# Optimization experiments

Hardware: AMD Instinct MI355X
Metric: run time of the kernel (lower is better)

## Reference

```python
import jax, jax.numpy as jnp
import numpy as np

D_MODEL = 1024
NUM_HEADS = 16


def setup_inputs() -> dict:
    key = jax.random.key(0)
    kx, kq, kk, kv, ko = jax.random.split(key, 5)
    B, S, D = 4, 2048, D_MODEL
    scale = 0.02
    x = jax.random.normal(kx, (B, S, D), dtype=jnp.float32)
    wq = jax.random.normal(kq, (D, D), dtype=jnp.float32) * scale
    wk = jax.random.normal(kk, (D, D), dtype=jnp.float32) * scale
    wv = jax.random.normal(kv, (D, D), dtype=jnp.float32) * scale
    wo = jax.random.normal(ko, (D, D), dtype=jnp.float32) * scale
    return {"x": x, "wq": wq, "wk": wk, "wv": wv, "wo": wo}


def reference(x, wq, wk, wv, wo):
    B, S, D = x.shape
    H = NUM_HEADS
    dk = D // H
    # projections: weight is [out, in] -> y = x @ W^T
    q = jnp.einsum('bsd,ed->bse', x, wq).reshape(B, S, H, dk).transpose(0, 2, 1, 3)
    k = jnp.einsum('bsd,ed->bse', x, wk).reshape(B, S, H, dk).transpose(0, 2, 1, 3)
    v = jnp.einsum('bsd,ed->bse', x, wv).reshape(B, S, H, dk).transpose(0, 2, 1, 3)
    # scaled dot-product attention with causal mask, [B,H,S,S]
    scores = jnp.einsum('bhqd,bhkd->bhqk', q, k) / jnp.sqrt(jnp.asarray(dk, x.dtype))
    causal = jnp.tril(jnp.ones((S, S), dtype=bool))
    scores = jnp.where(causal, scores, -jnp.inf)
    attn = jax.nn.softmax(scores, axis=-1)
    out = jnp.einsum('bhqk,bhkd->bhqd', attn, v)
    out = out.transpose(0, 2, 1, 3).reshape(B, S, D)
    return jnp.einsum('bse,de->bsd', out, wo)
```

## Files before the change

kernel.cpp:

```cpp
#include <hip/hip_runtime.h>

#define SEQ 2048
#define DM 1024
#define NH 16
#define DKH 64

typedef __attribute__((ext_vector_type(8))) short short8;
typedef __attribute__((ext_vector_type(4))) float f32x4;
typedef __attribute__((ext_vector_type(16))) float f32x16;
typedef __attribute__((ext_vector_type(2))) unsigned int u32x2;
typedef __attribute__((ext_vector_type(4))) unsigned int u32x4;

static __device__ __forceinline__ unsigned short f2b(float f) {
  unsigned int u = __float_as_uint(f);
  u += 0x7fffu + ((u >> 16) & 1u);
  return (unsigned short)(u >> 16);
}

static __device__ __forceinline__ short8 ldfrag_bf(const unsigned short* p) {
  return *reinterpret_cast<const short8*>(p);
}
static __device__ __forceinline__ short8 ldfrag_f32(const float* p) {
  const float4* q = reinterpret_cast<const float4*>(p);
  float4 a = q[0], b = q[1];
  short8 r;
  r[0] = (short)f2b(a.x); r[1] = (short)f2b(a.y);
  r[2] = (short)f2b(a.z); r[3] = (short)f2b(a.w);
  r[4] = (short)f2b(b.x); r[5] = (short)f2b(b.y);
  r[6] = (short)f2b(b.z); r[7] = (short)f2b(b.w);
  return r;
}

static __device__ __forceinline__ void gl_lds16(const void* g, void* l) {
  __builtin_amdgcn_global_load_lds(
      (const __attribute__((address_space(1))) unsigned int*)g,
      (__attribute__((address_space(3))) unsigned int*)l, 16, 0, 0);
}

__global__ __launch_bounds__(256) void zero_f32(float* __restrict__ p, int n4) {
  int i = blockIdx.x * 256 + threadIdx.x;
  if (i < n4) {
    float4 z = {0.f, 0.f, 0.f, 0.f};
    reinterpret_cast<float4*>(p)[i] = z;
  }
}

__global__ __launch_bounds__(256) void cast_all(const float* __restrict__ x,
                                                const float* __restrict__ a, const float* __restrict__ b,
                                                const float* __restrict__ c, const float* __restrict__ d,
                                                unsigned short* __restrict__ xo,
                                                unsigned short* __restrict__ oa, unsigned short* __restrict__ ob,
                                                unsigned short* __restrict__ oc, unsigned short* __restrict__ od) {
  int blk = blockIdx.x;
  if (blk < 8192) {
    int i = blk * 256 + threadIdx.x;
    float4 v = reinterpret_cast<const float4*>(x)[i];
    ushort4 o;
    o.x = f2b(v.x); o.y = f2b(v.y); o.z = f2b(v.z); o.w = f2b(v.w);
    reinterpret_cast<ushort4*>(xo)[i] = o;
  } else {
    blk -= 8192;
    int which = blk >> 10;
    int i = (blk & 1023) * 256 + threadIdx.x;
    const float* s = (which == 0) ? a : (which == 1) ? b : (which == 2) ? c : d;
    unsigned short* o = (which == 0) ? oa : (which == 1) ? ob : (which == 2) ? oc : od;
    float sc = (which == 0) ? 0.125f : 1.0f;
    float4 v = reinterpret_cast<const float4*>(s)[i];
    ushort4 u;
    u.x = f2b(v.x * sc); u.y = f2b(v.y * sc); u.z = f2b(v.z * sc); u.w = f2b(v.w * sc);
    reinterpret_cast<ushort4*>(o)[i] = u;
  }
}

__global__ __launch_bounds__(256) void gemm_qkv(const unsigned short* __restrict__ A,
                                                const unsigned short* __restrict__ Wq,
                                                const unsigned short* __restrict__ Wk,
                                                const unsigned short* __restrict__ Wv,
                                                unsigned short* __restrict__ Qb,
                                                unsigned short* __restrict__ Kb,
                                                unsigned short* __restrict__ Vt) {
  __shared__ char smem[49152];
  unsigned short* At = (unsigned short*)smem;
  unsigned short* Wt = (unsigned short*)(smem + 24576);
  int t = threadIdx.x;
  int lane = t & 63;
  int w = t >> 6;
  int l16 = lane & 15, q4 = lane >> 4;
  int mode = blockIdx.x % 3;
  int bid = blockIdx.x / 3;
  int mt = bid >> 3, nt = bid & 7;
  int m0 = mt * 128, n0 = nt * 128;
  int mw = (w & 1) * 64, nw = (w >> 1) * 64;
  const unsigned short* W = (mode == 0) ? Wq : (mode == 1) ? Wk : Wv;

  const f32x4 zero4 = {0.f, 0.f, 0.f, 0.f};
  f32x4 acc[4][4];
#pragma unroll
  for (int mi = 0; mi < 4; ++mi)
#pragma unroll
    for (int nj = 0; nj < 4; ++nj) acc[mi][nj] = zero4;

  int rl0 = t >> 2, cp = t & 3;
  int rl1 = rl0 + 64;
  int sw0 = ((cp - rl0 - (rl0 >> 2)) & 3) * 8;
  int sw1 = ((cp - rl1 - (rl1 >> 2)) & 3) * 8;
  const unsigned short* ga0 = A + (long)(m0 + rl0) * DM + sw0;
  const unsigned short* ga1 = A + (long)(m0 + rl1) * DM + sw1;
  const unsigned short* gw0 = W + (long)(n0 + rl0) * DM + sw0;
  const unsigned short* gw1 = W + (long)(n0 + rl1) * DM + sw1;
  char* lA = (char*)At + t * 16;
  char* lW = (char*)Wt + t * 16;

  int aoff[4], woff[4];
#pragma unroll
  for (int mi = 0; mi < 4; ++mi) {
    int r = mw + mi * 16 + l16;
    aoff[mi] = r * 32 + ((q4 + r + (r >> 2)) & 3) * 8;
  }
#pragma unroll
  for (int nj = 0; nj < 4; ++nj) {
    int r = nw + nj * 16 + l16;
    woff[nj] = r * 32 + ((q4 + r + (r >> 2)) & 3) * 8;
  }

  auto issue = [&](int boB) {
    gl_lds16(ga0, lA + boB); gl_lds16(ga1, lA + boB + 4096);
    gl_lds16(gw0, lW + boB); gl_lds16(gw1, lW + boB + 4096);
    ga0 += 32; ga1 += 32; gw0 += 32; gw1 += 32;
  };

  issue(0);
  issue(8192);
  __asm__ volatile("s_waitcnt vmcnt(4)" ::: "memory");
  __builtin_amdgcn_sched_barrier(0);
  __builtin_amdgcn_s_barrier();
  __builtin_amdgcn_sched_barrier(0);

  int cbB = 0, pbB = 16384;
  for (int ks = 0; ks < 32; ++ks) {
    if (ks < 30) issue(pbB);

    const unsigned short* Ab = (const unsigned short*)((char*)At + cbB);
    const unsigned short* Wb = (const unsigned short*)((char*)Wt + cbB);
    short8 af[4], wf[4];
#pragma unroll
    for (int mi = 0; mi < 4; ++mi) af[mi] = ldfrag_bf(Ab + aoff[mi]);
#pragma unroll
    for (int nj = 0; nj < 4; ++nj) wf[nj] = ldfrag_bf(Wb + woff[nj]);
#pragma unroll
    for (int mi = 0; mi < 4; ++mi)
#pragma unroll
      for (int nj = 0; nj < 4; ++nj)
        acc[mi][nj] = __builtin_amdgcn_mfma_f32_16x16x32_bf16(af[mi], wf[nj], acc[mi][nj], 0, 0, 0);

    if (ks < 31) {
      if (ks < 30) { __asm__ volatile("s_waitcnt vmcnt(4)" ::: "memory"); }
      else         { __asm__ volatile("s_waitcnt vmcnt(0)" ::: "memory"); }
      __builtin_amdgcn_sched_barrier(0);
      __builtin_amdgcn_s_barrier();
      __builtin_amdgcn_sched_barrier(0);
    }
    cbB += 8192; if (cbB == 24576) cbB = 0;
    pbB += 8192; if (pbB == 24576) pbB = 0;
  }

  if (mode != 2) {
    unsigned short* o = (mode == 0) ? Qb : Kb;
    int b = m0 >> 11;
    int h = (n0 + nw) >> 6;
    long bh0 = (long)(b * NH + h);
    unsigned short* op = o + (bh0 * SEQ + (m0 & 2047) + mw + q4 * 4) * DKH + l16;
#pragma unroll
    for (int mi = 0; mi < 4; ++mi)
#pragma unroll
      for (int nj = 0; nj < 4; ++nj)
#pragma unroll
        for (int r = 0; r < 4; ++r)
          op[mi * 1024 + r * 64 + nj * 16] = f2b(acc[mi][nj][r]);
  } else {
    __syncthreads();
    unsigned short* vle = (unsigned short*)(smem + w * 8192);
    unsigned int* vle32 = (unsigned int*)vle;
#pragma unroll
    for (int nj = 0; nj < 4; ++nj) {
      int d = nj * 16 + l16;
      int k8 = (d & 7) * 8;
#pragma unroll
      for (int mi = 0; mi < 4; ++mi)
#pragma unroll
        for (int r = 0; r < 4; r += 2) {
          int s = mi * 16 + q4 * 4 + r;
          unsigned int pk = (unsigned int)f2b(acc[mi][nj][r]) |
                            ((unsigned int)f2b(acc[mi][nj][r + 1]) << 16);
          vle32[d * 32 + ((s ^ k8) >> 1)] = pk;
        }
    }
    __asm__ volatile("s_waitcnt lgkmcnt(0)" ::: "memory");
    int b = m0 >> 11;
    int h = (n0 + nw) >> 6;
    long bh = (long)(b * NH + h);
    int sbase = (m0 + mw) & 2047;
    int dr_lo = lane >> 3, c = lane & 7;
    const unsigned short* vr = vle + dr_lo * 64 + (c ^ dr_lo) * 8;
    unsigned short* vtp = Vt + (bh * DKH + dr_lo) * SEQ + sbase + c * 8;
#pragma unroll
    for (int pass = 0; pass < 8; ++pass) {
      short8 vv = ldfrag_bf(vr + pass * 512);
      *reinterpret_cast<short8*>(vtp + (long)pass * 8 * SEQ) = vv;
    }
  }
}

__global__ __launch_bounds__(256) void gemm_o(const unsigned short* __restrict__ A,
                                              const unsigned short* __restrict__ W,
                                              float* __restrict__ outp) {
  __shared__ char smem[49152];
  unsigned short* At = (unsigned short*)smem;
  unsigned short* Wt = (unsigned short*)(smem + 24576);
  int t = threadIdx.x;
  int lane = t & 63;
  int w = t >> 6;
  int l16 = lane & 15, q4 = lane >> 4;
  int swz = (blockIdx.x & 7) * 64 + (blockIdx.x >> 3);
  int mt = swz >> 3, nt = swz & 7;
  int m0 = mt * 128, n0 = nt * 128;
  int mw = (w & 1) * 64, nw = (w >> 1) * 64;

  const f32x4 zero4 = {0.f, 0.f, 0.f, 0.f};
  f32x4 acc[4][4];
#pragma unroll
  for (int mi = 0; mi < 4; ++mi)
#pragma unroll
    for (int nj = 0; nj < 4; ++nj) acc[mi][nj] = zero4;

  int rl0 = t >> 2, cp = t & 3;
  int rl1 = rl0 + 64;
  int sw0 = ((cp - rl0 - (rl0 >> 2)) & 3) * 8;
  int sw1 = ((cp - rl1 - (rl1 >> 2)) & 3) * 8;
  int b0 = m0 >> 11;
  const unsigned short* ga0;
  const unsigned short* ga1;
  {
    int s0 = (m0 & 2047) + rl0;
    ga0 = A + (long)b0 * (NH * SEQ * DKH) + (long)s0 * DKH + sw0;
    int s1 = (m0 & 2047) + rl1;
    ga1 = A + (long)b0 * (NH * SEQ * DKH) + (long)s1 * DKH + sw1;
  }
  const unsigned short* gw0 = W + (long)(n0 + rl0) * DM + sw0;
  const unsigned short* gw1 = W + (long)(n0 + rl1) * DM + sw1;
  char* lA = (char*)At + t * 16;
  char* lW = (char*)Wt + t * 16;

  int aoff[4], woff[4];
#pragma unroll
  for (int mi = 0; mi < 4; ++mi) {
    int r = mw + mi * 16 + l16;
    aoff[mi] = r * 32 + ((q4 + r + (r >> 2)) & 3) * 8;
  }
#pragma unroll
  for (int nj = 0; nj < 4; ++nj) {
    int r = nw + nj * 16 + l16;
    woff[nj] = r * 32 + ((q4 + r + (r >> 2)) & 3) * 8;
  }

  int js = 0;
  auto issue = [&](int boB) {
    gl_lds16(ga0, lA + boB); gl_lds16(ga1, lA + boB + 4096);
    gl_lds16(gw0, lW + boB); gl_lds16(gw1, lW + boB + 4096);
    int adv = ((js & 1) == 0) ? 32 : (SEQ * DKH - 32);
    ga0 += adv; ga1 += adv; gw0 += 32; gw1 += 32;
    ++js;
  };

  issue(0);
  issue(8192);
  __asm__ volatile("s_waitcnt vmcnt(4)" ::: "memory");
  __builtin_amdgcn_sched_barrier(0);
  __builtin_amdgcn_s_barrier();
  __builtin_amdgcn_sched_barrier(0);

  int cbB = 0, pbB = 16384;
  for (int ks = 0; ks < 32; ++ks) {
    if (ks < 30) issue(pbB);

    const unsigned short* Ab = (const unsigned short*)((char*)At + cbB);
    const unsigned short* Wb = (const unsigned short*)((char*)Wt + cbB);
    short8 af[4], wf[4];
#pragma unroll
    for (int mi = 0; mi < 4; ++mi) af[mi] = ldfrag_bf(Ab + aoff[mi]);
#pragma unroll
    for (int nj = 0; nj < 4; ++nj) wf[nj] = ldfrag_bf(Wb + woff[nj]);
#pragma unroll
    for (int mi = 0; mi < 4; ++mi)
#pragma unroll
      for (int nj = 0; nj < 4; ++nj)
        acc[mi][nj] = __builtin_amdgcn_mfma_f32_16x16x32_bf16(af[mi], wf[nj], acc[mi][nj], 0, 0, 0);

    if (ks < 31) {
      if (ks < 30) { __asm__ volatile("s_waitcnt vmcnt(4)" ::: "memory"); }
      else         { __asm__ volatile("s_waitcnt vmcnt(0)" ::: "memory"); }
      __builtin_amdgcn_sched_barrier(0);
      __builtin_amdgcn_s_barrier();
      __builtin_amdgcn_sched_barrier(0);
    }
    cbB += 8192; if (cbB == 24576) cbB = 0;
    pbB += 8192; if (pbB == 24576) pbB = 0;
  }

  {
    float* op = outp + (long)(m0 + mw + q4 * 4) * DM + n0 + nw + l16;
#pragma unroll
    for (int mi = 0; mi < 4; ++mi)
#pragma unroll
      for (int nj = 0; nj < 4; ++nj)
#pragma unroll
        for (int r = 0; r < 4; ++r)
          op[(mi * 16 + r) * DM + nj * 16] = acc[mi][nj][r];
  }
}

template<int MODE, bool AF32, bool WF32>
__global__ __launch_bounds__(256) void gemm_s(const void* __restrict__ Ap,
                                              const void* __restrict__ Wp,
                                              void* __restrict__ outp) {
  int wid  = (blockIdx.x * 256 + threadIdx.x) >> 6;
  int lane = threadIdx.x & 63;
  int l16  = lane & 15, q4 = lane >> 4;
  int tn = wid & 15, tm = wid >> 4;
  int m0 = tm * 32, n0 = tn * 64;

  const float*          Af = (const float*)Ap;
  const unsigned short* Ab = (const unsigned short*)Ap;
  const float*          Wf = (const float*)Wp;
  const unsigned short* Wb = (const unsigned short*)Wp;

  const f32x4 zero4 = {0.f, 0.f, 0.f, 0.f};
  f32x4 acc[2][4];
#pragma unroll
  for (int mi = 0; mi < 2; ++mi)
#pragma unroll
    for (int j = 0; j < 4; ++j) acc[mi][j] = zero4;

  int wrow[4];
#pragma unroll
  for (int j = 0; j < 4; ++j) wrow[j] = (n0 + j * 16 + l16) * DM;
  int arow[2] = {0, 0};
  long abase[2] = {0, 0};
  if (MODE != 3) {
#pragma unroll
    for (int mi = 0; mi < 2; ++mi) arow[mi] = (m0 + mi * 16 + l16) * DM;
  } else {
    int b = m0 >> 11;
#pragma unroll
    for (int mi = 0; mi < 2; ++mi) {
      int srow = (m0 & 2047) + mi * 16 + l16;
      abase[mi] = (long)b * (NH * SEQ * DKH) + (long)srow * DKH;
    }
  }

#pragma unroll 2
  for (int ks = 0; ks < 32; ++ks) {
    int ko = ks * 32 + q4 * 8;
    short8 bfrag[4];
#pragma unroll
    for (int j = 0; j < 4; ++j) {
      if constexpr (WF32) bfrag[j] = ldfrag_f32(Wf + wrow[j] + ko);
      else                bfrag[j] = ldfrag_bf(Wb + wrow[j] + ko);
    }
    short8 afrag[2];
    if constexpr (MODE != 3) {
#pragma unroll
      for (int mi = 0; mi < 2; ++mi) {
        if constexpr (AF32) afrag[mi] = ldfrag_f32(Af + arow[mi] + ko);
        else                afrag[mi] = ldfrag_bf(Ab + arow[mi] + ko);
      }
    } else {
      int h = ko >> 6, e63 = ko & 63;
#pragma unroll
      for (int mi = 0; mi < 2; ++mi)
        afrag[mi] = ldfrag_bf(Ab + abase[mi] + (long)h * (SEQ * DKH) + e63);
    }
#pragma unroll
    for (int mi = 0; mi < 2; ++mi)
#pragma unroll
      for (int j = 0; j < 4; ++j)
        acc[mi][j] = __builtin_amdgcn_mfma_f32_16x16x32_bf16(afrag[mi], bfrag[j], acc[mi][j], 0, 0, 0);
  }

#pragma unroll
  for (int mi = 0; mi < 2; ++mi) {
#pragma unroll
    for (int j = 0; j < 4; ++j) {
#pragma unroll
      for (int r = 0; r < 4; ++r) {
        float v = acc[mi][j][r];
        int m = m0 + mi * 16 + q4 * 4 + r;
        int n = n0 + j * 16 + l16;
        if constexpr (MODE == 3) {
          reinterpret_cast<float*>(outp)[(long)m * DM + n] = v;
        } else {
          int b = m >> 11, s = m & 2047;
          int h = n >> 6, d = n & 63;
          long bh = (long)(b * NH + h);
          unsigned short* o = reinterpret_cast<unsigned short*>(outp);
          if constexpr (MODE == 0)      o[(bh * SEQ + s) * DKH + d] = f2b(v * 0.125f);
          else if constexpr (MODE == 1) o[(bh * SEQ + s) * DKH + d] = f2b(v);
          else                          o[(bh * DKH + d) * SEQ + s] = f2b(v);
        }
      }
    }
  }
}

__global__ __launch_bounds__(256, 4) void attn_k(const unsigned short* __restrict__ Kbuf,
                                                 const unsigned short* __restrict__ Vt,
                                                 const unsigned short* __restrict__ Qbuf,
                                                 unsigned short* __restrict__ Obuf) {
  __shared__ unsigned short Kt[2][64 * 64];
  __shared__ unsigned short Vts[2][64 * 64];

  int t = threadIdx.x;
  int lane = t & 63;
  int w = t >> 6;
  int l31 = lane & 31, hi = lane >> 5;
  int qb = 15 - (blockIdx.x >> 6);
  int bh = blockIdx.x & 63;
  int q0 = qb * 128;
  int qw0 = q0 + w * 32;

  const unsigned short* Qh = Qbuf + (long)bh * (SEQ * DKH);
  const unsigned short* Kh = Kbuf + (long)bh * (SEQ * DKH);
  const unsigned short* Vh = Vt   + (long)bh * (DKH * SEQ);

  short8 qf[4];
#pragma unroll
  for (int dt = 0; dt < 4; ++dt)
    qf[dt] = ldfrag_bf(Qh + (long)(qw0 + l31) * DKH + dt * 16 + hi * 8);

  f32x16 om[2];
#pragma unroll
  for (int dv = 0; dv < 2; ++dv)
#pragma unroll
    for (int r = 0; r < 16; ++r) om[dv][r] = 0.f;
  float lsum = 0.f;

  int koff[2][4];
#pragma unroll
  for (int sub = 0; sub < 2; ++sub) {
    int kr = sub * 32 + l31;
#pragma unroll
    for (int dt = 0; dt < 4; ++dt)
      koff[sub][dt] = kr * 64 + ((dt * 2 + hi + kr + (kr >> 3)) & 7) * 8;
  }
  int voff[2][4];
#pragma unroll
  for (int dv = 0; dv < 2; ++dv) {
    int dr = dv * 32 + l31;
#pragma unroll
    for (int kc = 0; kc < 4; ++kc)
      voff[dv][kc] = dr * 64 + ((kc * 2 + hi + dr + (dr >> 3)) & 7) * 8;
  }

  int rl0 = t >> 3, cp = t & 7;
  int rl1 = rl0 + 32;
  int sw0 = ((cp - rl0 - (rl0 >> 3)) & 7) * 8;
  int sw1 = ((cp - rl1 - (rl1 >> 3)) & 7) * 8;
  const unsigned short* kp0 = Kh + (long)rl0 * DKH + sw0;
  const unsigned short* kp1 = Kh + (long)rl1 * DKH + sw1;
  const unsigned short* vp0 = Vh + (long)rl0 * SEQ + sw0;
  const unsigned short* vp1 = Vh + (long)rl1 * SEQ + sw1;
  char* lK = (char*)Kt + t * 16;
  char* lV = (char*)Vts + t * 16;

  int nk = 2 * qb + 2;
  gl_lds16(kp0, lK); gl_lds16(kp1, lK + 4096);
  gl_lds16(vp0, lV); gl_lds16(vp1, lV + 4096);

  for (int it = 0; it < nk; ++it) {
    __syncthreads();
    if (it + 1 < nk) {
      kp0 += 64 * DKH; kp1 += 64 * DKH; vp0 += 64; vp1 += 64;
      int bo = ((it + 1) & 1) * 8192;
      gl_lds16(kp0, lK + bo); gl_lds16(kp1, lK + bo + 4096);
      gl_lds16(vp0, lV + bo); gl_lds16(vp1, lV + bo + 4096);
    }

    int k0 = it * 64;
    if (k0 <= qw0 + 31) {
      const unsigned short* KT = Kt[0] + (it & 1) * 4096;
      const unsigned short* VT = Vts[0] + (it & 1) * 4096;

#pragma unroll
      for (int sub = 0; sub < 2; ++sub) {
        int ksb = k0 + sub * 32;
        if (ksb <= qw0 + 31) {
          f32x16 s;
#pragma unroll
          for (int r = 0; r < 16; ++r) s[r] = 0.f;
#pragma unroll
          for (int dt = 0; dt < 4; ++dt) {
            short8 kf = ldfrag_bf(KT + koff[sub][dt]);
            s = __builtin_amdgcn_mfma_f32_32x32x16_bf16(kf, qf[dt], s, 0, 0, 0);
          }

          bool needmask = (ksb + 31 > qw0);
          int qr = qw0 + l31;
          unsigned int pk[4][2];
#pragma unroll
          for (int r = 0; r < 16; r += 2) {
            float p0 = __expf(s[r]);
            float p1 = __expf(s[r + 1]);
            if (needmask) {
              int key = ksb + (r & 3) + 8 * (r >> 2) + 4 * hi;
              p0 = (key <= qr) ? p0 : 0.f;
              p1 = (key + 1 <= qr) ? p1 : 0.f;
            }
            unsigned int u0 = __float_as_uint(p0) & 0xffff0000u;
            unsigned int u1 = __float_as_uint(p1) & 0xffff0000u;
            lsum += __uint_as_float(u0) + __uint_as_float(u1);
            pk[r >> 2][(r >> 1) & 1] = (u0 >> 16) | u1;
          }

#pragma unroll
          for (int c = 0; c < 2; ++c) {
            u32x2 r0 = __builtin_amdgcn_permlane32_swap(pk[2 * c][0], pk[2 * c + 1][0], false, false);
            u32x2 r1 = __builtin_amdgcn_permlane32_swap(pk[2 * c][1], pk[2 * c + 1][1], false, false);
            u32x4 pw;
            pw.x = r0.x; pw.y = r1.x; pw.z = r0.y; pw.w = r1.y;
            short8 pa = __builtin_bit_cast(short8, pw);
            int kc = sub * 2 + c;
#pragma unroll
            for (int dv = 0; dv < 2; ++dv) {
              short8 vf = ldfrag_bf(VT + voff[dv][kc]);
              om[dv] = __builtin_amdgcn_mfma_f32_32x32x16_bf16(pa, vf, om[dv], 0, 0, 0);
            }
          }
        }
      }
    }
  }

  u32x2 lz = __builtin_amdgcn_permlane32_swap(__float_as_uint(lsum), __float_as_uint(lsum),
                                              false, false);
  float inv = 1.f / (__uint_as_float(lz.x) + __uint_as_float(lz.y));

  long obase = (long)bh * (SEQ * DKH);
#pragma unroll
  for (int r = 0; r < 16; ++r) {
    int qrow = (r & 3) + 8 * (r >> 2) + 4 * hi;
    float invq = __shfl(inv, qrow);
    long rowb = obase + (long)(qw0 + qrow) * DKH + l31;
    Obuf[rowb]      = f2b(om[0][r] * invq);
    Obuf[rowb + 32] = f2b(om[1][r] * invq);
  }
}

extern "C" void kernel_launch(void* const* d_in, const int* in_sizes, int n_in,
                              void* d_out, int out_size, void* d_ws, size_t ws_size,
                              hipStream_t stream) {
  const float* x  = (const float*)d_in[0];
  const float* wq = (const float*)d_in[1];
  const float* wk = (const float*)d_in[2];
  const float* wv = (const float*)d_in[3];
  const float* wo = (const float*)d_in[4];

  unsigned short* Qb = (unsigned short*)d_out;
  unsigned short* Kb = Qb + 8388608;

  if (ws_size >= 41943040ull) {
    unsigned short* xb  = (unsigned short*)d_ws;
    unsigned short* wqb = xb + 8388608;
    unsigned short* wkb = wqb + 1048576;
    unsigned short* wvb = wkb + 1048576;
    unsigned short* wob = wvb + 1048576;
    unsigned short* Vt  = wob + 1048576;
    unsigned short* Ob  = xb;

    cast_all<<<12288, 256, 0, stream>>>(x, wq, wk, wv, wo, xb, wqb, wkb, wvb, wob);

    gemm_qkv<<<1536, 256, 0, stream>>>(xb, wqb, wkb, wvb, Qb, Kb, Vt);
    attn_k<<<1024, 256, 0, stream>>>(Kb, Vt, Qb, Ob);
    gemm_o<<<512, 256, 0, stream>>>(Ob, wob, (float*)d_out);
  } else if (ws_size >= 33554432ull) {
    unsigned short* Vt = (unsigned short*)d_ws;
    unsigned short* Ob = Vt + 8388608;

    gemm_s<0, true, true><<<1024, 256, 0, stream>>>(x, wq, Qb);
    gemm_s<1, true, true><<<1024, 256, 0, stream>>>(x, wk, Kb);
    gemm_s<2, true, true><<<1024, 256, 0, stream>>>(x, wv, Vt);
    attn_k<<<1024, 256, 0, stream>>>(Kb, Vt, Qb, Ob);
    gemm_s<3, false, true><<<1024, 256, 0, stream>>>(Ob, wo, d_out);
  } else {
    zero_f32<<<8192, 256, 0, stream>>>((float*)d_out, 2097152);
  }
}
```

Measured before the change: 248.6 us.

## Fuse Q, K and V projections per block to share the activation tile

Each block of the QKV projection kernel now computes all three outputs (Q, K and V) for its 128x128 tile, instead of launching a separate block per projection. Every A-tile fragment loaded into shared memory is reused across three weight tiles, which cuts global and LDS traffic for the activations to a third. The prologue and pipeline change from a triple-buffered scheme with hand-tuned vmcnt waits to a double-buffered 64KB scheme gated by __syncthreads. This triples accumulator register pressure (192 fp32 per lane) and reduces the grid to 512 blocks, which risks spills, lower occupancy and less load/compute overlap.

```diff
diff --git a/kernel.cpp b/kernel.cpp
--- a/kernel.cpp
+++ b/kernel.cpp
@@ -72,44 +72,38 @@
   }
 }
 
-__global__ __launch_bounds__(256) void gemm_qkv(const unsigned short* __restrict__ A,
-                                                const unsigned short* __restrict__ Wq,
-                                                const unsigned short* __restrict__ Wk,
-                                                const unsigned short* __restrict__ Wv,
-                                                unsigned short* __restrict__ Qb,
-                                                unsigned short* __restrict__ Kb,
-                                                unsigned short* __restrict__ Vt) {
-  __shared__ char smem[49152];
-  unsigned short* At = (unsigned short*)smem;
-  unsigned short* Wt = (unsigned short*)(smem + 24576);
+__global__ __launch_bounds__(256, 2) void gemm_qkv(const unsigned short* __restrict__ A,
+                                                   const unsigned short* __restrict__ Wq,
+                                                   const unsigned short* __restrict__ Wk,
+                                                   const unsigned short* __restrict__ Wv,
+                                                   unsigned short* __restrict__ Qb,
+                                                   unsigned short* __restrict__ Kb,
+                                                   unsigned short* __restrict__ Vt) {
+  __shared__ char smem[65536];
   int t = threadIdx.x;
   int lane = t & 63;
   int w = t >> 6;
   int l16 = lane & 15, q4 = lane >> 4;
-  int mode = blockIdx.x % 3;
-  int bid = blockIdx.x / 3;
-  int mt = bid >> 3, nt = bid & 7;
+  int mt = blockIdx.x >> 3, nt = blockIdx.x & 7;
   int m0 = mt * 128, n0 = nt * 128;
   int mw = (w & 1) * 64, nw = (w >> 1) * 64;
-  const unsigned short* W = (mode == 0) ? Wq : (mode == 1) ? Wk : Wv;
 
   const f32x4 zero4 = {0.f, 0.f, 0.f, 0.f};
-  f32x4 acc[4][4];
-#pragma unroll
-  for (int mi = 0; mi < 4; ++mi)
-#pragma unroll
-    for (int nj = 0; nj < 4; ++nj) acc[mi][nj] = zero4;
+  f32x4 acc[3][4][4];
+#pragma unroll
+  for (int md = 0; md < 3; ++md)
+#pragma unroll
+    for (int mi = 0; mi < 4; ++mi)
+#pragma unroll
+      for (int nj = 0; nj < 4; ++nj) acc[md][mi][nj] = zero4;
 
   int rl0 = t >> 2, cp = t & 3;
-  int rl1 = rl0 + 64;
-  int sw0 = ((cp - rl0 - (rl0 >> 2)) & 3) * 8;
-  int sw1 = ((cp - rl1 - (rl1 >> 2)) & 3) * 8;
-  const unsigned short* ga0 = A + (long)(m0 + rl0) * DM + sw0;
-  const unsigned short* ga1 = A + (long)(m0 + rl1) * DM + sw1;
-  const unsigned short* gw0 = W + (long)(n0 + rl0) * DM + sw0;
-  const unsigned short* gw1 = W + (long)(n0 + rl1) * DM + sw1;
-  char* lA = (char*)At + t * 16;
-  char* lW = (char*)Wt + t * 16;
+  int sw = ((cp - rl0 - (rl0 >> 2)) & 3) * 8;
+  const unsigned short* ga = A  + (long)(m0 + rl0) * DM + sw;
+  const unsigned short* gq = Wq + (long)(n0 + rl0) * DM + sw;
+  const unsigned short* gk = Wk + (long)(n0 + rl0) * DM + sw;
+  const unsigned short* gv = Wv + (long)(n0 + rl0) * DM + sw;
+  char* ldst = smem + t * 16;
 
   int aoff[4], woff[4];
 #pragma unroll
@@ -123,86 +117,81 @@
     woff[nj] = r * 32 + ((q4 + r + (r >> 2)) & 3) * 8;
   }
 
-  auto issue = [&](int boB) {
-    gl_lds16(ga0, lA + boB); gl_lds16(ga1, lA + boB + 4096);
-    gl_lds16(gw0, lW + boB); gl_lds16(gw1, lW + boB + 4096);
-    ga0 += 32; ga1 += 32; gw0 += 32; gw1 += 32;
+  auto issue = [&](int bufB) {
+    gl_lds16(ga,           ldst + bufB);
+    gl_lds16(ga + 64 * DM, ldst + bufB + 4096);
+    gl_lds16(gq,           ldst + bufB + 8192);
+    gl_lds16(gq + 64 * DM, ldst + bufB + 12288);
+    gl_lds16(gk,           ldst + bufB + 16384);
+    gl_lds16(gk + 64 * DM, ldst + bufB + 20480);
+    gl_lds16(gv,           ldst + bufB + 24576);
+    gl_lds16(gv + 64 * DM, ldst + bufB + 28672);
+    ga += 32; gq += 32; gk += 32; gv += 32;
   };
 
   issue(0);
-  issue(8192);
-  __asm__ volatile("s_waitcnt vmcnt(4)" ::: "memory");
-  __builtin_amdgcn_sched_barrier(0);
-  __builtin_amdgcn_s_barrier();
-  __builtin_amdgcn_sched_barrier(0);
-
-  int cbB = 0, pbB = 16384;
   for (int ks = 0; ks < 32; ++ks) {
-    if (ks < 30) issue(pbB);
-
-    const unsigned short* Ab = (const unsigned short*)((char*)At + cbB);
-    const unsigned short* Wb = (const unsigned short*)((char*)Wt + cbB);
-    short8 af[4], wf[4];
-#pragma unroll
-    for (int mi = 0; mi < 4; ++mi) af[mi] = ldfrag_bf(Ab + aoff[mi]);
-#pragma unroll
-    for (int nj = 0; nj < 4; ++nj) wf[nj] = ldfrag_bf(Wb + woff[nj]);
+    __syncthreads();
+    if (ks + 1 < 32) issue(((ks + 1) & 1) * 32768);
+
+    const unsigned short* base = (const unsigned short*)(smem + (ks & 1) * 32768);
+    short8 af[4];
+#pragma unroll
+    for (int mi = 0; mi < 4; ++mi) af[mi] = ldfrag_bf(base + aoff[mi]);
+#pragma unroll
+    for (int md = 0; md < 3; ++md) {
+      const unsigned short* Wb = base + 4096 + md * 4096;
+#pragma unroll
+      for (int nj = 0; nj < 4; ++nj) {
+        short8 wfj = ldfrag_bf(Wb + woff[nj]);
+#pragma unroll
+        for (int mi = 0; mi < 4; ++mi)
+          acc[md][mi][nj] = __builtin_amdgcn_mfma_f32_16x16x32_bf16(af[mi], wfj, acc[md][mi][nj], 0, 0, 0);
+      }
+    }
+  }
+
+  int b = m0 >> 11;
+  int h = (n0 + nw) >> 6;
+  long bh0 = (long)(b * NH + h);
+  long obase = (bh0 * SEQ + (m0 & 2047) + mw + q4 * 4) * DKH + l16;
+  {
+    unsigned short* opq = Qb + obase;
+    unsigned short* opk = Kb + obase;
 #pragma unroll
     for (int mi = 0; mi < 4; ++mi)
 #pragma unroll
       for (int nj = 0; nj < 4; ++nj)
-        acc[mi][nj] = __builtin_amdgcn_mfma_f32_16x16x32_bf16(af[mi], wf[nj], acc[mi][nj], 0, 0, 0);
-
-    if (ks < 31) {
-      if (ks < 30) { __asm__ volatile("s_waitcnt vmcnt(4)" ::: "memory"); }
-      else         { __asm__ volatile("s_waitcnt vmcnt(0)" ::: "memory"); }
-      __builtin_amdgcn_sched_barrier(0);
-      __builtin_amdgcn_s_barrier();
-      __builtin_amdgcn_sched_barrier(0);
-    }
-    cbB += 8192; if (cbB == 24576) cbB = 0;
-    pbB += 8192; if (pbB == 24576) pbB = 0;
-  }
-
-  if (mode != 2) {
-    unsigned short* o = (mode == 0) ? Qb : Kb;
-    int b = m0 >> 11;
-    int h = (n0 + nw) >> 6;
-    long bh0 = (long)(b * NH + h);
-    unsigned short* op = o + (bh0 * SEQ + (m0 & 2047) + mw + q4 * 4) * DKH + l16;
+#pragma unroll
+        for (int r = 0; r < 4; ++r) {
+          opq[mi * 1024 + r * 64 + nj * 16] = f2b(acc[0][mi][nj][r]);
+          opk[mi * 1024 + r * 64 + nj * 16] = f2b(acc[1][mi][nj][r]);
+        }
+  }
+
+  __syncthreads();
+  unsigned short* vle = (unsigned short*)(smem + w * 8192);
+  unsigned int* vle32 = (unsigned int*)vle;
+#pragma unroll
+  for (int nj = 0; nj < 4; ++nj) {
+    int d = nj * 16 + l16;
+    int k8 = (d & 7) * 8;
 #pragma unroll
     for (int mi = 0; mi < 4; ++mi)
 #pragma unroll
-      for (int nj = 0; nj < 4; ++nj)
-#pragma unroll
-        for (int r = 0; r < 4; ++r)
-          op[mi * 1024 + r * 64 + nj * 16] = f2b(acc[mi][nj][r]);
-  } else {
-    __syncthreads();
-    unsigned short* vle = (unsigned short*)(smem + w * 8192);
-    unsigned int* vle32 = (unsigned int*)vle;
-#pragma unroll
-    for (int nj = 0; nj < 4; ++nj) {
-      int d = nj * 16 + l16;
-      int k8 = (d & 7) * 8;
-#pragma unroll
-      for (int mi = 0; mi < 4; ++mi)
-#pragma unroll
-        for (int r = 0; r < 4; r += 2) {
-          int s = mi * 16 + q4 * 4 + r;
-          unsigned int pk = (unsigned int)f2b(acc[mi][nj][r]) |
-                            ((unsigned int)f2b(acc[mi][nj][r + 1]) << 16);
-          vle32[d * 32 + ((s ^ k8) >> 1)] = pk;
-        }
-    }
-    __asm__ volatile("s_waitcnt lgkmcnt(0)" ::: "memory");
-    int b = m0 >> 11;
-    int h = (n0 + nw) >> 6;
-    long bh = (long)(b * NH + h);
+      for (int r = 0; r < 4; r += 2) {
+        int s = mi * 16 + q4 * 4 + r;
+        unsigned int pk = (unsigned int)f2b(acc[2][mi][nj][r]) |
+                          ((unsigned int)f2b(acc[2][mi][nj][r + 1]) << 16);
+        vle32[d * 32 + ((s ^ k8) >> 1)] = pk;
+      }
+  }
+  __asm__ volatile("s_waitcnt lgkmcnt(0)" ::: "memory");
+  {
     int sbase = (m0 + mw) & 2047;
     int dr_lo = lane >> 3, c = lane & 7;
     const unsigned short* vr = vle + dr_lo * 64 + (c ^ dr_lo) * 8;
-    unsigned short* vtp = Vt + (bh * DKH + dr_lo) * SEQ + sbase + c * 8;
+    unsigned short* vtp = Vt + (bh0 * DKH + dr_lo) * SEQ + sbase + c * 8;
 #pragma unroll
     for (int pass = 0; pass < 8; ++pass) {
       short8 vv = ldfrag_bf(vr + pass * 512);
@@ -578,7 +567,7 @@
 
     cast_all<<<12288, 256, 0, stream>>>(x, wq, wk, wv, wo, xb, wqb, wkb, wvb, wob);
 
-    gemm_qkv<<<1536, 256, 0, stream>>>(xb, wqb, wkb, wvb, Qb, Kb, Vt);
+    gemm_qkv<<<512, 256, 0, stream>>>(xb, wqb, wkb, wvb, Qb, Kb, Vt);
     attn_k<<<1024, 256, 0, stream>>>(Kb, Vt, Qb, Ob);
     gemm_o<<<512, 256, 0, stream>>>(Ob, wob, (float*)d_out);
   } else if (ws_size >= 33554432ull) {
```

Measured after the change: 232.9 us. 1.07x faster.
